# Optimization experiments

Measured on AMD Instinct MI355X. Metric: run time of the kernel, lower is better.

The kernel has to match this reference:

```python
import jax, jax.numpy as jnp
import numpy as np

B, C, H, W = 4, 256, 64, 64
DQK = C // 4


def setup_inputs() -> dict:
    key = jax.random.key(0)
    ks = jax.random.split(key, 5)
    s = 0.05
    x = jax.random.normal(ks[0], (B, C, H, W), dtype=jnp.float32)
    Wq = jax.random.normal(ks[1], (DQK, C), dtype=jnp.float32) * s
    Wk = jax.random.normal(ks[2], (DQK, C), dtype=jnp.float32) * s
    Wv = jax.random.normal(ks[3], (C, C), dtype=jnp.float32) * s
    bq = jnp.zeros((DQK,), jnp.float32)
    bk = jnp.zeros((DQK,), jnp.float32)
    bv = jnp.zeros((C,), jnp.float32)
    gamma = jnp.zeros((1,), jnp.float32)
    return {"x": x, "Wq": Wq, "bq": bq, "Wk": Wk, "bk": bk,
            "Wv": Wv, "bv": bv, "gamma": gamma}


def reference(x, Wq, bq, Wk, bk, Wv, bv, gamma):
    b, c, h, w = x.shape
    n = h * w
    xf = x.reshape(b, c, n)                      # [B, C, N]
    # 1x1 convs == per-pixel linear projections
    q = jnp.einsum('dc,bcn->bnd', Wq, xf) + bq   # [B, N, Dqk]
    k = jnp.einsum('dc,bcn->bdn', Wk, xf) + bk[None, :, None]  # [B, Dqk, N]
    v = jnp.einsum('ec,bcn->ben', Wv, xf) + bv[None, :, None]  # [B, C, N]
    energy = jnp.einsum('bnd,bdm->bnm', q, k)    # [B, N, N]
    attn = jax.nn.softmax(energy, axis=-1)       # softmax over keys
    # out[b,c,i] = sum_j v[b,c,j] * attn[b,i,j]
    out = jnp.einsum('bcj,bij->bci', v, attn)    # [B, C, N]
    out = out.reshape(b, c, h, w)
    return gamma * out + x
```

## Files before the change

### kernel.cpp

```cpp
#include <hip/hip_runtime.h>

#define B_ 4
#define C_ 256
#define N_ 4096
#define D_ 64

typedef __bf16 bf16x8 __attribute__((ext_vector_type(8)));
typedef float floatx4 __attribute__((ext_vector_type(4)));
typedef unsigned short ushort8v __attribute__((ext_vector_type(8)));
typedef unsigned short ushort4v __attribute__((ext_vector_type(4)));
typedef unsigned short ushort2v __attribute__((ext_vector_type(2)));

static __device__ __forceinline__ unsigned short f2bf(float f) {
    unsigned int u = __builtin_bit_cast(unsigned int, f);
    u += 0x7fffu + ((u >> 16) & 1u);
    return (unsigned short)(u >> 16);
}
static __device__ __forceinline__ float bf2f(unsigned short h) {
    unsigned int u = ((unsigned int)h) << 16;
    return __builtin_bit_cast(float, u);
}

#define GLOAD16(gp, lp)                                                      \
    __builtin_amdgcn_global_load_lds(                                        \
        (const __attribute__((address_space(1))) void*)(gp),                 \
        (__attribute__((address_space(3))) void*)(lp), 16, 0, 0)

__global__ __launch_bounds__(256) void convert_w(
    const float* __restrict__ Wq, const float* __restrict__ Wk,
    const float* __restrict__ Wv, unsigned short* __restrict__ WbfA)
{
    int tid = blockIdx.x * 256 + threadIdx.x;
    int p0  = tid * 4;
    int j0   = p0 & 7;
    int lane = (p0 >> 3) & 63;
    int sidx = p0 >> 9;
    int ft = sidx >> 3, ks = sidx & 7;
    int m  = lane & 15, g = lane >> 4;
    int f  = 16*ft + m;
    int c  = 32*ks + 8*g + j0;
    const float* src = (f < 64)  ? (Wq + (size_t)f * C_)
                     : (f < 128) ? (Wk + (size_t)(f - 64) * C_)
                                 : (Wv + (size_t)(f - 128) * C_);
    float4 v = *(const float4*)(src + c);
    ushort4v u;
    u[0] = f2bf(v.x); u[1] = f2bf(v.y); u[2] = f2bf(v.z); u[3] = f2bf(v.w);
    *(ushort4v*)(WbfA + p0) = u;
}

__global__ __launch_bounds__(256, 3) void proj_kernel(
    const float* __restrict__ x, const unsigned short* __restrict__ WbfA,
    const float* __restrict__ bq, const float* __restrict__ bk,
    const float* __restrict__ bv,
    unsigned short* __restrict__ Qg, unsigned short* __restrict__ Kg,
    unsigned short* __restrict__ Vg)
{
    __shared__ __align__(16) unsigned short smem[64 * 264];
    unsigned short* xs = smem;
    unsigned short* Lt = smem;

    const int n0 = blockIdx.x * 64;
    const int f0 = blockIdx.y * 128;
    const int b  = blockIdx.z;
    const int t  = threadIdx.x;
    const int w  = t >> 6;
    const int lane = t & 63;
    const int g  = lane >> 4;
    const int m  = lane & 15;

#pragma unroll
    for (int k = 0; k < 8; ++k) {
        int e  = t + 256 * k;
        int cp = e >> 4;
        int c  = 2 * cp;
        int n4 = (e & 15) * 4;
        float4 v0 = *(const float4*)(x + ((size_t)b*C_ + c    )*N_ + n0 + n4);
        float4 v1 = *(const float4*)(x + ((size_t)b*C_ + c + 1)*N_ + n0 + n4);
        float a0[4] = {v0.x, v0.y, v0.z, v0.w};
        float a1[4] = {v1.x, v1.y, v1.z, v1.w};
#pragma unroll
        for (int j = 0; j < 4; ++j) {
            int n = n4 + j;
            ushort2v u2;
            u2[0] = f2bf(a0[j]);
            u2[1] = f2bf(a1[j]);
            *(ushort2v*)&xs[n*264 + (((c >> 3) ^ (n & 7)) << 3) + (c & 7)] = u2;
        }
    }

    float bias_[2][4];
#pragma unroll
    for (int mt = 0; mt < 2; ++mt)
#pragma unroll
        for (int r = 0; r < 4; ++r) {
            int fg = f0 + 32*w + 16*mt + 4*g + r;
            bias_[mt][r] = (fg < 64) ? bq[fg]
                         : (fg < 128) ? bk[fg - 64] : bv[fg - 128];
        }

    const unsigned short* Wa0 = WbfA + (size_t)(((f0 >> 4) + 2*w    )*8)*512
                              + lane*8;
    const unsigned short* Wa1 = WbfA + (size_t)(((f0 >> 4) + 2*w + 1)*8)*512
                              + lane*8;

    floatx4 acc[2][4];
#pragma unroll
    for (int mt = 0; mt < 2; ++mt)
#pragma unroll
        for (int nt = 0; nt < 4; ++nt) acc[mt][nt] = (floatx4){0.f,0.f,0.f,0.f};

    __syncthreads();

#pragma unroll
    for (int ks = 0; ks < 8; ++ks) {
        bf16x8 af[2];
        af[0] = *(const bf16x8*)(Wa0 + ks*512);
        af[1] = *(const bf16x8*)(Wa1 + ks*512);
#pragma unroll
        for (int nt = 0; nt < 4; ++nt) {
            int n = 16*nt + m;
            bf16x8 bfr = *(const bf16x8*)
                &xs[n*264 + (((4*ks + g) ^ (n & 7)) << 3)];
#pragma unroll
            for (int mt = 0; mt < 2; ++mt)
                acc[mt][nt] = __builtin_amdgcn_mfma_f32_16x16x32_bf16(
                                  af[mt], bfr, acc[mt][nt], 0, 0, 0);
        }
    }

    __syncthreads();

#pragma unroll
    for (int mt = 0; mt < 2; ++mt)
#pragma unroll
        for (int nt = 0; nt < 4; ++nt)
#pragma unroll
            for (int r = 0; r < 4; ++r)
                Lt[(32*w + 16*mt + 4*g + r)*72 + 16*nt + m] =
                    f2bf(acc[mt][nt][r] + bias_[mt][r]);
    __syncthreads();

    if (f0 == 0) {
#pragma unroll
        for (int k = 0; k < 4; ++k) {
            int e   = t + 256 * k;
            int fq0 = (e >> 6) * 8;
            int nl  = e & 63;
            ushort8v u;
#pragma unroll
            for (int j = 0; j < 8; ++j) u[j] = Lt[(fq0 + j)*72 + nl];
            unsigned short* dst = (fq0 < 64)
                ? (Qg + ((size_t)b*N_ + n0 + nl)*D_ + fq0)
                : (Kg + ((size_t)b*N_ + n0 + nl)*D_ + (fq0 - 64));
            *(ushort8v*)dst = u;
        }
    } else {
        const int cb = f0 - 128;
#pragma unroll
        for (int k = 0; k < 4; ++k) {
            int e  = t + 256 * k;
            int fr = e >> 3;
            int n8 = (e & 7) * 8;
            ushort8v u = *(const ushort8v*)&Lt[fr*72 + n8];
            *(ushort8v*)(Vg + ((size_t)b*C_ + cb + fr)*N_ + n0 + n8) = u;
        }
    }
}

__global__ __launch_bounds__(256, 2) void flash_kernel(
    const unsigned short* __restrict__ Qg, const unsigned short* __restrict__ Kg,
    const unsigned short* __restrict__ Vg,
    unsigned short* __restrict__ Opart, float* __restrict__ ML)
{
    __shared__ __align__(16) unsigned short Vlds[32 * 512];
    __shared__ __align__(16) unsigned short Klds[2][8 * 512];
    __shared__ __align__(16) unsigned short PA[8 * 64 * 8];
    __shared__ float AL[64];

    const int g8   = blockIdx.x;
    const int tile = blockIdx.y;
    const int half = g8 & 1;
    const int b    = g8 >> 1;
    const int n0   = tile * 64;
    const int t    = threadIdx.x;
    const int w    = t >> 6;
    const int lane = t & 63;
    const int g    = lane >> 4;
    const int m    = lane & 15;

    const unsigned short* Qb = Qg + ((size_t)b*N_ + n0)*D_;
    const unsigned short* Kb = Kg + (size_t)b*N_*D_;
    const unsigned short* Vb = Vg + (size_t)b*C_*N_;

    const int cstart = half * 32;
    const int cend   = cstart + 32;

    bf16x8 qf[2];
#pragma unroll
    for (int ks = 0; ks < 2; ++ks)
        qf[ks] = *(const bf16x8*)(Qb + (size_t)(16*w + m)*D_ + 32*ks + 8*g);

    floatx4 accO[4][4];
#pragma unroll
    for (int rt = 0; rt < 4; ++rt)
#pragma unroll
        for (int ct = 0; ct < 4; ++ct)
            accO[rt][ct] = (floatx4){0.f, 0.f, 0.f, 0.f};

    float mrow = -1e30f, lrow = 0.f;

#pragma unroll
    for (int u = 0; u < 2; ++u) {
        const unsigned short* gp =
            Kb + (size_t)(cstart*64 + 16*w + m)*D_ + 32*u + 8*g;
        GLOAD16(gp, &Klds[0][(2*w + u) * 512]);
    }
    __syncthreads();

    for (int t64 = cstart; t64 < cend; ++t64) {
        const int j0 = t64 * 64;
        const int kb = (t64 - cstart) & 1;

#pragma unroll
        for (int u = 0; u < 8; ++u) {
            int sidx = 8*w + u;
            int ks   = sidx >> 4;
            int cb   = sidx & 15;
            const unsigned short* gp =
                Vb + (size_t)(16*cb + m)*N_ + j0 + 32*ks + 8*g;
            GLOAD16(gp, &Vlds[sidx * 512]);
        }
        if (t64 + 1 < cend) {
#pragma unroll
            for (int u = 0; u < 2; ++u) {
                const unsigned short* gp =
                    Kb + (size_t)((t64+1)*64 + 16*w + m)*D_ + 32*u + 8*g;
                GLOAD16(gp, &Klds[kb ^ 1][(2*w + u) * 512]);
            }
        }

        floatx4 accST[4];
#pragma unroll
        for (int jt = 0; jt < 4; ++jt) accST[jt] = (floatx4){0.f,0.f,0.f,0.f};
#pragma unroll
        for (int ks = 0; ks < 2; ++ks)
#pragma unroll
            for (int jt = 0; jt < 4; ++jt) {
                bf16x8 kfr = *(const bf16x8*)
                    &Klds[kb][(jt*2 + ks)*512 + lane*8];
                accST[jt] = __builtin_amdgcn_mfma_f32_16x16x32_bf16(
                                kfr, qf[ks], accST[jt], 0, 0, 0);
            }

        float mx = -1e30f;
#pragma unroll
        for (int jt = 0; jt < 4; ++jt)
#pragma unroll
            for (int r = 0; r < 4; ++r) mx = fmaxf(mx, accST[jt][r]);
        mx = fmaxf(mx, __shfl_xor(mx, 16));
        mx = fmaxf(mx, __shfl_xor(mx, 32));
        float mnew  = fmaxf(mrow, mx);
        float alpha = __expf(mrow - mnew);
        mrow = mnew;
        float p[4][4];
        float rs = 0.f;
#pragma unroll
        for (int jt = 0; jt < 4; ++jt)
#pragma unroll
            for (int r = 0; r < 4; ++r) {
                float e = __expf(accST[jt][r] - mnew);
                p[jt][r] = e;
                rs += e;
            }
        rs += __shfl_xor(rs, 16);
        rs += __shfl_xor(rs, 32);
        lrow = lrow * alpha + rs;

        if (g == 0) AL[16*w + m] = alpha;

#pragma unroll
        for (int jt = 0; jt < 4; ++jt) {
            ushort4v u;
#pragma unroll
            for (int r = 0; r < 4; ++r) u[r] = f2bf(p[jt][r]);
            int frag = (w*2 + (jt >> 1))*64 + 16*(2*(jt & 1) + (g >> 1)) + m;
            *(ushort4v*)&PA[frag*8 + 4*(g & 1)] = u;
        }

        __syncthreads();

#pragma unroll
        for (int rt = 0; rt < 4; ++rt) {
            floatx4 a4 = *(const floatx4*)&AL[16*rt + 4*g];
#pragma unroll
            for (int ct = 0; ct < 4; ++ct)
                accO[rt][ct] *= a4;
        }
#pragma unroll
        for (int ks = 0; ks < 2; ++ks) {
            bf16x8 pf[4];
#pragma unroll
            for (int rt = 0; rt < 4; ++rt)
                pf[rt] = *(const bf16x8*)&PA[((rt*2 + ks)*64 + lane)*8];
#pragma unroll
            for (int ct = 0; ct < 4; ++ct) {
                int sidx = ks*16 + 4*w + ct;
                bf16x8 vfrag = *(const bf16x8*)&Vlds[sidx*512 + lane*8];
#pragma unroll
                for (int rt = 0; rt < 4; ++rt)
                    accO[rt][ct] = __builtin_amdgcn_mfma_f32_16x16x32_bf16(
                                       pf[rt], vfrag, accO[rt][ct], 0, 0, 0);
            }
        }

        __syncthreads();
    }

    const size_t tbase = ((size_t)(half*B_ + b)*64 + tile);
    unsigned short* Ob = Opart + tbase * (C_ * 64);
    float* ml = ML + tbase * 128;

    if (g == 0) {
        ml[16*w + m]      = mrow;
        ml[64 + 16*w + m] = lrow;
    }

#pragma unroll
    for (int rt = 0; rt < 4; ++rt)
#pragma unroll
        for (int ct = 0; ct < 4; ++ct) {
            int c = 64*w + 16*ct + m;
            ushort4v u4;
#pragma unroll
            for (int r = 0; r < 4; ++r) u4[r] = f2bf(accO[rt][ct][r]);
            *(ushort4v*)(Ob + (size_t)c*64 + 16*rt + 4*g) = u4;
        }
}

__global__ __launch_bounds__(256) void combine_kernel(
    const unsigned short* __restrict__ Opart, const float* __restrict__ ML,
    const float* __restrict__ x, const float* __restrict__ gamma,
    float* __restrict__ out)
{
    __shared__ float sc0[64], sc1[64];
    const int tile  = blockIdx.x;
    const int chalf = blockIdx.y;
    const int b     = blockIdx.z;
    const int n0    = tile * 64;
    const int t     = threadIdx.x;

    if (t < 64) {
        const float* ml0 = ML + ((size_t)(0*B_ + b)*64 + tile)*128;
        const float* ml1 = ML + ((size_t)(1*B_ + b)*64 + tile)*128;
        float m0 = ml0[t], l0 = ml0[64 + t];
        float m1 = ml1[t], l1 = ml1[64 + t];
        float M  = fmaxf(m0, m1);
        float f0 = __expf(m0 - M), f1 = __expf(m1 - M);
        float L  = f0*l0 + f1*l1;
        float gm = gamma[0];
        sc0[t] = gm * f0 / L;
        sc1[t] = gm * f1 / L;
    }
    __syncthreads();

    const int nq = t & 15;
    const float* xb = x   + (size_t)b*C_*N_;
    float*       ob = out + (size_t)b*C_*N_;
    const unsigned short* O0 = Opart + ((size_t)(0*B_ + b)*64 + tile)*(C_*64);
    const unsigned short* O1 = Opart + ((size_t)(1*B_ + b)*64 + tile)*(C_*64);

    float s0[4], s1[4];
#pragma unroll
    for (int k = 0; k < 4; ++k) { s0[k] = sc0[4*nq + k]; s1[k] = sc1[4*nq + k]; }

#pragma unroll 4
    for (int i = 0; i < 8; ++i) {
        int c = 128*chalf + 16*i + (t >> 4);
        float4 x4 = *(const float4*)(xb + (size_t)c*N_ + n0 + 4*nq);
        ushort4v a4 = *(const ushort4v*)(O0 + (size_t)c*64 + 4*nq);
        ushort4v b4 = *(const ushort4v*)(O1 + (size_t)c*64 + 4*nq);
        float4 y;
        y.x = s0[0]*bf2f(a4[0]) + s1[0]*bf2f(b4[0]) + x4.x;
        y.y = s0[1]*bf2f(a4[1]) + s1[1]*bf2f(b4[1]) + x4.y;
        y.z = s0[2]*bf2f(a4[2]) + s1[2]*bf2f(b4[2]) + x4.z;
        y.w = s0[3]*bf2f(a4[3]) + s1[3]*bf2f(b4[3]) + x4.w;
        *(float4*)(ob + (size_t)c*N_ + n0 + 4*nq) = y;
    }
}

extern "C" void kernel_launch(void* const* d_in, const int* in_sizes, int n_in,
                              void* d_out, int out_size, void* d_ws, size_t ws_size,
                              hipStream_t stream) {
    const float* x     = (const float*)d_in[0];
    const float* Wq    = (const float*)d_in[1];
    const float* bq    = (const float*)d_in[2];
    const float* Wk    = (const float*)d_in[3];
    const float* bk    = (const float*)d_in[4];
    const float* Wv    = (const float*)d_in[5];
    const float* bv    = (const float*)d_in[6];
    const float* gamma = (const float*)d_in[7];
    float* out = (float*)d_out;

    unsigned short* Qg = (unsigned short*)d_ws;
    unsigned short* Kg = Qg + (size_t)B_*N_*D_;
    unsigned short* Vg = Kg + (size_t)B_*N_*D_;
    unsigned short* Op = Vg + (size_t)B_*C_*N_;
    float* ML = (float*)(Op + (size_t)2*B_*64*C_*64);
    unsigned short* WbfA = (unsigned short*)(ML + (size_t)2*B_*64*128);

    convert_w<<<dim3(96), 256, 0, stream>>>(Wq, Wk, Wv, WbfA);
    proj_kernel<<<dim3(64, 3, 4), 256, 0, stream>>>(x, WbfA, bq, bk, bv,
                                                    Qg, Kg, Vg);
    flash_kernel<<<dim3(8, 64), 256, 0, stream>>>(Qg, Kg, Vg, Op, ML);
    combine_kernel<<<dim3(64, 2, 4), 256, 0, stream>>>(Op, ML, x, gamma, out);
}
```

Baseline: 177.6 us.

## Double flash query tile to 128 rows with 512-thread blocks sharing K/V tiles

The flash kernel now processes 128 query rows per block using 8 waves: two query halves by four channel quarters. Each staged K and V tile in LDS is reused across twice as many queries, which halves the global K/V traffic per query. Partial outputs, row statistics and the combine kernel are re-indexed to the 128-wide tile. The cost is half as many blocks (256) for the GPU's CUs. The launch bound of 512 threads with 4 blocks per CU constrains register allocation and may cause spills.

```diff
diff --git a/kernel.cpp b/kernel.cpp
--- a/kernel.cpp
+++ b/kernel.cpp
@@ -167,26 +167,28 @@
     }
 }
 
-__global__ __launch_bounds__(256, 2) void flash_kernel(
+__global__ __launch_bounds__(512, 4) void flash_kernel(
     const unsigned short* __restrict__ Qg, const unsigned short* __restrict__ Kg,
     const unsigned short* __restrict__ Vg,
     unsigned short* __restrict__ Opart, float* __restrict__ ML)
 {
     __shared__ __align__(16) unsigned short Vlds[32 * 512];
     __shared__ __align__(16) unsigned short Klds[2][8 * 512];
-    __shared__ __align__(16) unsigned short PA[8 * 64 * 8];
-    __shared__ float AL[64];
+    __shared__ __align__(16) unsigned short PA[16 * 64 * 8];
+    __shared__ float AL[128];
 
     const int g8   = blockIdx.x;
     const int tile = blockIdx.y;
     const int half = g8 & 1;
     const int b    = g8 >> 1;
-    const int n0   = tile * 64;
+    const int n0   = tile * 128;
     const int t    = threadIdx.x;
     const int w    = t >> 6;
     const int lane = t & 63;
     const int g    = lane >> 4;
     const int m    = lane & 15;
+    const int qh   = w >> 2;
+    const int cq   = w & 3;
 
     const unsigned short* Qb = Qg + ((size_t)b*N_ + n0)*D_;
     const unsigned short* Kb = Kg + (size_t)b*N_*D_;
@@ -209,11 +211,10 @@
 
     float mrow = -1e30f, lrow = 0.f;
 
-#pragma unroll
-    for (int u = 0; u < 2; ++u) {
+    {
         const unsigned short* gp =
-            Kb + (size_t)(cstart*64 + 16*w + m)*D_ + 32*u + 8*g;
-        GLOAD16(gp, &Klds[0][(2*w + u) * 512]);
+            Kb + (size_t)(cstart*64 + 16*(w >> 1) + m)*D_ + 32*(w & 1) + 8*g;
+        GLOAD16(gp, &Klds[0][w * 512]);
     }
     __syncthreads();
 
@@ -222,8 +223,8 @@
         const int kb = (t64 - cstart) & 1;
 
 #pragma unroll
-        for (int u = 0; u < 8; ++u) {
-            int sidx = 8*w + u;
+        for (int u = 0; u < 4; ++u) {
+            int sidx = 4*w + u;
             int ks   = sidx >> 4;
             int cb   = sidx & 15;
             const unsigned short* gp =
@@ -231,12 +232,9 @@
             GLOAD16(gp, &Vlds[sidx * 512]);
         }
         if (t64 + 1 < cend) {
-#pragma unroll
-            for (int u = 0; u < 2; ++u) {
-                const unsigned short* gp =
-                    Kb + (size_t)((t64+1)*64 + 16*w + m)*D_ + 32*u + 8*g;
-                GLOAD16(gp, &Klds[kb ^ 1][(2*w + u) * 512]);
-            }
+            const unsigned short* gp =
+                Kb + (size_t)((t64+1)*64 + 16*(w >> 1) + m)*D_ + 32*(w & 1) + 8*g;
+            GLOAD16(gp, &Klds[kb ^ 1][w * 512]);
         }
 
         floatx4 accST[4];
@@ -291,7 +289,7 @@
 
 #pragma unroll
         for (int rt = 0; rt < 4; ++rt) {
-            floatx4 a4 = *(const floatx4*)&AL[16*rt + 4*g];
+            floatx4 a4 = *(const floatx4*)&AL[64*qh + 16*rt + 4*g];
 #pragma unroll
             for (int ct = 0; ct < 4; ++ct)
                 accO[rt][ct] *= a4;
@@ -301,10 +299,11 @@
             bf16x8 pf[4];
 #pragma unroll
             for (int rt = 0; rt < 4; ++rt)
-                pf[rt] = *(const bf16x8*)&PA[((rt*2 + ks)*64 + lane)*8];
+                pf[rt] = *(const bf16x8*)
+                    &PA[(((4*qh + rt)*2 + ks)*64 + lane)*8];
 #pragma unroll
             for (int ct = 0; ct < 4; ++ct) {
-                int sidx = ks*16 + 4*w + ct;
+                int sidx = ks*16 + 4*cq + ct;
                 bf16x8 vfrag = *(const bf16x8*)&Vlds[sidx*512 + lane*8];
 #pragma unroll
                 for (int rt = 0; rt < 4; ++rt)
@@ -316,24 +315,24 @@
         __syncthreads();
     }
 
-    const size_t tbase = ((size_t)(half*B_ + b)*64 + tile);
-    unsigned short* Ob = Opart + tbase * (C_ * 64);
-    float* ml = ML + tbase * 128;
+    const size_t tbase = ((size_t)(half*B_ + b)*32 + tile);
+    unsigned short* Ob = Opart + tbase * (C_ * 128);
+    float* ml = ML + tbase * 256;
 
     if (g == 0) {
-        ml[16*w + m]      = mrow;
-        ml[64 + 16*w + m] = lrow;
+        ml[16*w + m]       = mrow;
+        ml[128 + 16*w + m] = lrow;
     }
 
 #pragma unroll
     for (int rt = 0; rt < 4; ++rt)
 #pragma unroll
         for (int ct = 0; ct < 4; ++ct) {
-            int c = 64*w + 16*ct + m;
+            int c = 64*cq + 16*ct + m;
             ushort4v u4;
 #pragma unroll
             for (int r = 0; r < 4; ++r) u4[r] = f2bf(accO[rt][ct][r]);
-            *(ushort4v*)(Ob + (size_t)c*64 + 16*rt + 4*g) = u4;
+            *(ushort4v*)(Ob + (size_t)c*128 + 64*qh + 16*rt + 4*g) = u4;
         }
 }
 
@@ -342,18 +341,18 @@
     const float* __restrict__ x, const float* __restrict__ gamma,
     float* __restrict__ out)
 {
-    __shared__ float sc0[64], sc1[64];
+    __shared__ float sc0[128], sc1[128];
     const int tile  = blockIdx.x;
     const int chalf = blockIdx.y;
     const int b     = blockIdx.z;
-    const int n0    = tile * 64;
+    const int n0    = tile * 128;
     const int t     = threadIdx.x;
 
-    if (t < 64) {
-        const float* ml0 = ML + ((size_t)(0*B_ + b)*64 + tile)*128;
-        const float* ml1 = ML + ((size_t)(1*B_ + b)*64 + tile)*128;
-        float m0 = ml0[t], l0 = ml0[64 + t];
-        float m1 = ml1[t], l1 = ml1[64 + t];
+    if (t < 128) {
+        const float* ml0 = ML + ((size_t)(0*B_ + b)*32 + tile)*256;
+        const float* ml1 = ML + ((size_t)(1*B_ + b)*32 + tile)*256;
+        float m0 = ml0[t], l0 = ml0[128 + t];
+        float m1 = ml1[t], l1 = ml1[128 + t];
         float M  = fmaxf(m0, m1);
         float f0 = __expf(m0 - M), f1 = __expf(m1 - M);
         float L  = f0*l0 + f1*l1;
@@ -363,22 +362,23 @@
     }
     __syncthreads();
 
-    const int nq = t & 15;
+    const int nq = t & 31;
+    const int cl = t >> 5;
     const float* xb = x   + (size_t)b*C_*N_;
     float*       ob = out + (size_t)b*C_*N_;
-    const unsigned short* O0 = Opart + ((size_t)(0*B_ + b)*64 + tile)*(C_*64);
-    const unsigned short* O1 = Opart + ((size_t)(1*B_ + b)*64 + tile)*(C_*64);
+    const unsigned short* O0 = Opart + ((size_t)(0*B_ + b)*32 + tile)*(C_*128);
+    const unsigned short* O1 = Opart + ((size_t)(1*B_ + b)*32 + tile)*(C_*128);
 
     float s0[4], s1[4];
 #pragma unroll
     for (int k = 0; k < 4; ++k) { s0[k] = sc0[4*nq + k]; s1[k] = sc1[4*nq + k]; }
 
 #pragma unroll 4
-    for (int i = 0; i < 8; ++i) {
-        int c = 128*chalf + 16*i + (t >> 4);
+    for (int i = 0; i < 16; ++i) {
+        int c = 128*chalf + 8*i + cl;
         float4 x4 = *(const float4*)(xb + (size_t)c*N_ + n0 + 4*nq);
-        ushort4v a4 = *(const ushort4v*)(O0 + (size_t)c*64 + 4*nq);
-        ushort4v b4 = *(const ushort4v*)(O1 + (size_t)c*64 + 4*nq);
+        ushort4v a4 = *(const ushort4v*)(O0 + (size_t)c*128 + 4*nq);
+        ushort4v b4 = *(const ushort4v*)(O1 + (size_t)c*128 + 4*nq);
         float4 y;
         y.x = s0[0]*bf2f(a4[0]) + s1[0]*bf2f(b4[0]) + x4.x;
         y.y = s0[1]*bf2f(a4[1]) + s1[1]*bf2f(b4[1]) + x4.y;
@@ -405,12 +405,12 @@
     unsigned short* Kg = Qg + (size_t)B_*N_*D_;
     unsigned short* Vg = Kg + (size_t)B_*N_*D_;
     unsigned short* Op = Vg + (size_t)B_*C_*N_;
-    float* ML = (float*)(Op + (size_t)2*B_*64*C_*64);
-    unsigned short* WbfA = (unsigned short*)(ML + (size_t)2*B_*64*128);
+    float* ML = (float*)(Op + (size_t)2*B_*32*C_*128);
+    unsigned short* WbfA = (unsigned short*)(ML + (size_t)2*B_*32*256);
 
     convert_w<<<dim3(96), 256, 0, stream>>>(Wq, Wk, Wv, WbfA);
     proj_kernel<<<dim3(64, 3, 4), 256, 0, stream>>>(x, WbfA, bq, bk, bv,
                                                     Qg, Kg, Vg);
-    flash_kernel<<<dim3(8, 64), 256, 0, stream>>>(Qg, Kg, Vg, Op, ML);
-    combine_kernel<<<dim3(64, 2, 4), 256, 0, stream>>>(Op, ML, x, gamma, out);
-}
+    flash_kernel<<<dim3(8, 32), 512, 0, stream>>>(Qg, Kg, Vg, Op, ML);
+    combine_kernel<<<dim3(32, 2, 4), 256, 0, stream>>>(Op, ML, x, gamma, out);
+}
```

After: 249.3 us. 40.3% more time.
